# Performance work log

Measured on AMD Instinct MI355X. Metric: run time of the kernel, lower is better.

The kernel has to match this reference:

```python
import jax, jax.numpy as jnp
import numpy as np

B, C, VC, H, W = 4, 256, 128, 64, 64


def setup_inputs() -> dict:
    key = jax.random.key(0)
    kx, kq, kk, kv = jax.random.split(key, 4)
    # Conv2d 1x1 no-bias weights are just [out_channels, in_channels] matrices.
    s = 1.0 / np.sqrt(C)
    return {
        "x": jax.random.normal(kx, (B, C, H, W), dtype=jnp.float32),
        "Wq": jax.random.uniform(kq, (VC, C), minval=-s, maxval=s, dtype=jnp.float32),
        "Wk": jax.random.uniform(kk, (VC, C), minval=-s, maxval=s, dtype=jnp.float32),
        "Wv": jax.random.uniform(kv, (VC, C), minval=-s, maxval=s, dtype=jnp.float32),
    }


def reference(x, Wq, Wk, Wv):
    # 1x1 convs == per-pixel channel GEMMs
    Q = jnp.einsum('bchw,dc->bdhw', x, Wq)  # [B, VC, H, W]
    K = jnp.einsum('bchw,dc->bdhw', x, Wk)
    V = jnp.einsum('bchw,dc->bdhw', x, Wv)
    b, d, h, w = Q.shape
    # affinity over all spatial pairs: [B, H, W, H, W]
    aff = jnp.einsum('bdij,bdkl->bijkl', Q, K).reshape(b, h, w, h * w)
    aff = jax.nn.softmax(aff, axis=3).reshape(b, h, w, h, w)
    # attention-weighted aggregation of values
    out = jnp.einsum('bijkl,bdkl->bdij', aff, V)  # [B, VC, H, W]
    return out
```

## Files before the change

kernel.cpp:

```cpp
#include <hip/hip_runtime.h>
#include <hip/hip_bf16.h>

#define B_ 4
#define C_ 256
#define D_ 128
#define N_ 4096

typedef float f32x4 __attribute__((ext_vector_type(4)));
typedef short bf16x8 __attribute__((ext_vector_type(8)));
typedef short s16x4 __attribute__((ext_vector_type(4)));
typedef unsigned short u16;
typedef unsigned int u32;

__device__ __forceinline__ u16 f2bf(float f) {
  unsigned u = __float_as_uint(f);
  u += 0x7fffu + ((u >> 16) & 1u);
  return (u16)(u >> 16);
}
__device__ __forceinline__ float bf2f(u16 v) {
  return __uint_as_float(((u32)v) << 16);
}
__device__ __forceinline__ u32 cvt_pk_bf16(float a, float b) {
  u32 r;
  asm("v_cvt_pk_bf16_f32 %0, %1, %2" : "=v"(r) : "v"(a), "v"(b));
  return r;
}

__global__ __launch_bounds__(256) void castw_kernel(
    const float* __restrict__ Wq, const float* __restrict__ Wk,
    const float* __restrict__ Wv, u16* __restrict__ Whi,
    u16* __restrict__ Wlo) {
  const int i = blockIdx.x * 256 + threadIdx.x;
  const int m = i >> 13;
  const int j = (i & 8191) * 4;
  const float* src = (m == 0) ? Wq : (m == 1) ? Wk : Wv;
  const float scale = (m == 0) ? 1.44269504f : 1.0f;
  const float4 v = *(const float4*)(src + j);
  const float vv[4] = {v.x * scale, v.y * scale, v.z * scale, v.w * scale};
  s16x4 h, l;
#pragma unroll
  for (int k = 0; k < 4; ++k) {
    const u16 hb = f2bf(vv[k]);
    h[k] = (short)hb;
    l[k] = (short)f2bf(vv[k] - bf2f(hb));
  }
  *(s16x4*)&Whi[m * 32768 + j] = h;
  *(s16x4*)&Wlo[m * 32768 + j] = l;
}

__global__ __launch_bounds__(256, 3) void proj_kernel(
    const float* __restrict__ x, const u16* __restrict__ Whi,
    const u16* __restrict__ Wlo, u16* __restrict__ Qo, u16* __restrict__ Ko,
    u16* __restrict__ Vt) {
  __shared__ __align__(16) u16 xs_h[32 * 256];
  __shared__ __align__(16) u16 xs_l[32 * 256];

  const int n0 = blockIdx.x * 32;
  const int b = blockIdx.y;
  const int z = blockIdx.z;
  const int t = threadIdx.x;
  const int w = t >> 6, lane = t & 63, g = lane >> 4, c = lane & 15;

  {
    const float* xb = x + ((size_t)b * C_) * N_ + n0;
#pragma unroll
    for (int r = 0; r < 8; ++r) {
      const int id = r * 256 + t;
      const int cr = id >> 3, nq = (id & 7) * 4;
      const float4 v = *(const float4*)(xb + (size_t)cr * N_ + nq);
      const float vv[4] = {v.x, v.y, v.z, v.w};
#pragma unroll
      for (int k2 = 0; k2 < 4; ++k2) {
        const int idx2 = (nq + k2) * 256 + (cr ^ (((nq + k2) & 7) << 3));
        const u16 hb = f2bf(vv[k2]);
        xs_h[idx2] = hb;
        xs_l[idx2] = f2bf(vv[k2] - bf2f(hb));
      }
    }
  }
  __syncthreads();

  if (w < 2) {
    const size_t wo = (size_t)w * 32768;
    u16* __restrict__ O = (w == 0 ? Qo : Ko) + (size_t)b * N_ * D_;
#pragma unroll 1
    for (int dti = 0; dti < 4; ++dti) {
      const int dt = z * 4 + dti;
      f32x4 a0 = {0.f, 0.f, 0.f, 0.f};
      f32x4 a1 = {0.f, 0.f, 0.f, 0.f};
#pragma unroll 1
      for (int kcb = 0; kcb < 2; ++kcb) {
        bf16x8 wfh[4], wfl[4];
#pragma unroll
        for (int j = 0; j < 4; ++j) {
          const size_t off = wo + (size_t)(dt * 16 + c) * 256 +
                             (kcb * 4 + j) * 32 + g * 8;
          wfh[j] = *(const bf16x8*)&Whi[off];
          wfl[j] = *(const bf16x8*)&Wlo[off];
        }
#pragma unroll
        for (int j = 0; j < 4; ++j) {
          const int kc = kcb * 4 + j;
          const int col = (kc * 32 + g * 8) ^ ((c & 7) << 3);
          const bf16x8 xh0 = *(const bf16x8*)&xs_h[c * 256 + col];
          const bf16x8 xl0 = *(const bf16x8*)&xs_l[c * 256 + col];
          const bf16x8 xh1 = *(const bf16x8*)&xs_h[(16 + c) * 256 + col];
          const bf16x8 xl1 = *(const bf16x8*)&xs_l[(16 + c) * 256 + col];
          a0 = __builtin_amdgcn_mfma_f32_16x16x32_bf16(xh0, wfh[j], a0, 0, 0, 0);
          a0 = __builtin_amdgcn_mfma_f32_16x16x32_bf16(xh0, wfl[j], a0, 0, 0, 0);
          a0 = __builtin_amdgcn_mfma_f32_16x16x32_bf16(xl0, wfh[j], a0, 0, 0, 0);
          a1 = __builtin_amdgcn_mfma_f32_16x16x32_bf16(xh1, wfh[j], a1, 0, 0, 0);
          a1 = __builtin_amdgcn_mfma_f32_16x16x32_bf16(xh1, wfl[j], a1, 0, 0, 0);
          a1 = __builtin_amdgcn_mfma_f32_16x16x32_bf16(xl1, wfh[j], a1, 0, 0, 0);
        }
      }
#pragma unroll
      for (int i = 0; i < 4; ++i) {
        O[(size_t)(n0 + g * 4 + i) * D_ + dt * 16 + c] = f2bf(a0[i]);
        O[(size_t)(n0 + 16 + g * 4 + i) * D_ + dt * 16 + c] = f2bf(a1[i]);
      }
    }
  } else {
    const size_t wo = (size_t)2 * 32768;
    const int d0 = (w - 2) * 64 + z * 32;
    u16* __restrict__ O = Vt + (size_t)b * D_ * N_;
#pragma unroll 1
    for (int dti = 0; dti < 2; ++dti) {
      const int dr = d0 + dti * 16;
      f32x4 a0 = {0.f, 0.f, 0.f, 0.f};
      f32x4 a1 = {0.f, 0.f, 0.f, 0.f};
#pragma unroll 1
      for (int kcb = 0; kcb < 2; ++kcb) {
        bf16x8 wfh[4], wfl[4];
#pragma unroll
        for (int j = 0; j < 4; ++j) {
          const size_t off =
              wo + (size_t)(dr + c) * 256 + (kcb * 4 + j) * 32 + g * 8;
          wfh[j] = *(const bf16x8*)&Whi[off];
          wfl[j] = *(const bf16x8*)&Wlo[off];
        }
#pragma unroll
        for (int j = 0; j < 4; ++j) {
          const int kc = kcb * 4 + j;
          const int col = (kc * 32 + g * 8) ^ ((c & 7) << 3);
          const bf16x8 xh0 = *(const bf16x8*)&xs_h[c * 256 + col];
          const bf16x8 xl0 = *(const bf16x8*)&xs_l[c * 256 + col];
          const bf16x8 xh1 = *(const bf16x8*)&xs_h[(16 + c) * 256 + col];
          const bf16x8 xl1 = *(const bf16x8*)&xs_l[(16 + c) * 256 + col];
          a0 = __builtin_amdgcn_mfma_f32_16x16x32_bf16(wfh[j], xh0, a0, 0, 0, 0);
          a0 = __builtin_amdgcn_mfma_f32_16x16x32_bf16(wfl[j], xh0, a0, 0, 0, 0);
          a0 = __builtin_amdgcn_mfma_f32_16x16x32_bf16(wfh[j], xl0, a0, 0, 0, 0);
          a1 = __builtin_amdgcn_mfma_f32_16x16x32_bf16(wfh[j], xh1, a1, 0, 0, 0);
          a1 = __builtin_amdgcn_mfma_f32_16x16x32_bf16(wfl[j], xh1, a1, 0, 0, 0);
          a1 = __builtin_amdgcn_mfma_f32_16x16x32_bf16(wfh[j], xl1, a1, 0, 0, 0);
        }
      }
#pragma unroll
      for (int i = 0; i < 4; ++i) {
        O[(size_t)(dr + g * 4 + i) * N_ + n0 + c] = f2bf(a0[i]);
        O[(size_t)(dr + g * 4 + i) * N_ + n0 + 16 + c] = f2bf(a1[i]);
      }
    }
  }
}

__device__ __forceinline__ int kIdx(int row, int col) {
  return row * 128 + (col ^ ((row & 7) << 3));
}
__device__ __forceinline__ int vIdx(int d, int col) {
  return d * 64 + (col ^ ((d & 7) << 3));
}
__device__ __forceinline__ int kprm(int q) {
  const int ct = q >> 2, qq = q & 3;
  return ((ct >> 1) << 5) +
         (((qq >> 1) == (ct & 1)) ? (qq << 3) : (((qq ^ 2) << 3) + 4));
}

__global__ __launch_bounds__(256, 2) void attn_kernel(
    const u16* __restrict__ Q, const u16* __restrict__ K,
    const u16* __restrict__ Vt, u16* __restrict__ op,
    float* __restrict__ mb, float* __restrict__ lb,
    float* __restrict__ outf, int qt, int rem, int S) {
  __shared__ __align__(16) u16 lds_k[2][64 * 128];
  __shared__ __align__(16) u16 lds_vt[2][128 * 64];

  const int L = blockIdx.x;
  int qx, b, sid;
  if (((B_ * S) & 7) == 0) {
    const int gpx = (B_ * S) >> 3;
    const int xcd = L & 7, idx = L >> 3;
    const int grp = xcd * gpx + (idx >> 5);
    qx = idx & 31;
    b = grp / S;
    sid = grp - b * S;
  } else {
    qx = L & 31;
    const int r2 = L >> 5;
    b = r2 % B_;
    sid = r2 / B_;
  }
  const int q0 = qx * 128;
  const int NT = qt + (sid < rem ? 1 : 0);
  const int t0 = sid * qt + (sid < rem ? sid : rem);
  const int k0 = t0 * 64;
  const int t = threadIdx.x;
  const int w = t >> 6, lane = t & 63, g = lane >> 4, c = lane & 15;
  const int qw = q0 + w * 32;
  const bool ghi = (g & 2) != 0;

  const u16* __restrict__ Qb = Q + (size_t)b * N_ * D_;
  const u16* __restrict__ Kb = K + (size_t)b * N_ * D_;
  const u16* __restrict__ Vb = Vt + (size_t)b * D_ * N_;

  bf16x8 qf[2][4];
#pragma unroll
  for (int qh = 0; qh < 2; ++qh)
#pragma unroll
    for (int kc = 0; kc < 4; ++kc)
      qf[qh][kc] =
          *(const bf16x8*)&Qb[(size_t)(qw + qh * 16 + c) * D_ + kc * 32 + g * 8];

  f32x4 acc[8][2];
  f32x4 accl[2];
#pragma unroll
  for (int dt = 0; dt < 8; ++dt)
#pragma unroll
    for (int qh = 0; qh < 2; ++qh) acc[dt][qh] = (f32x4){0.f, 0.f, 0.f, 0.f};
  accl[0] = (f32x4){0.f, 0.f, 0.f, 0.f};
  accl[1] = (f32x4){0.f, 0.f, 0.f, 0.f};
  float mrow[2] = {-3.0e38f, -3.0e38f};
  const float THR = 11.5415603f;

  bf16x8 onesv;
#pragma unroll
  for (int j = 0; j < 8; ++j) onesv[j] = (short)0x3F80;

  bf16x8 krg[8], vrg[8];
  auto load_pair = [&](int kbase) {
#pragma unroll
    for (int h = 0; h < 2; ++h)
#pragma unroll
      for (int i = 0; i < 4; ++i) {
        const int idx = i * 256 + t;
        const int kb2 = kbase + h * 64;
        krg[h * 4 + i] =
            *(const bf16x8*)&Kb[(size_t)(kb2 + (idx >> 4)) * D_ + (idx & 15) * 8];
        vrg[h * 4 + i] =
            *(const bf16x8*)&Vb[(size_t)(idx >> 3) * N_ + kb2 + (idx & 7) * 8];
      }
  };
  load_pair(k0);

  auto proc = [&](const u16* kb, const u16* vb) {
    f32x4 s[4][2];
#pragma unroll
    for (int ct = 0; ct < 4; ++ct)
#pragma unroll
      for (int qh = 0; qh < 2; ++qh) s[ct][qh] = (f32x4){0.f, 0.f, 0.f, 0.f};
    __builtin_amdgcn_s_setprio(1);
#pragma unroll
    for (int kc = 0; kc < 4; ++kc) {
#pragma unroll
      for (int ct = 0; ct < 4; ++ct) {
        const bf16x8 kf = *(const bf16x8*)&kb[kIdx(ct * 16 + c, kc * 32 + g * 8)];
        s[ct][0] = __builtin_amdgcn_mfma_f32_16x16x32_bf16(kf, qf[0][kc], s[ct][0], 0, 0, 0);
        s[ct][1] = __builtin_amdgcn_mfma_f32_16x16x32_bf16(kf, qf[1][kc], s[ct][1], 0, 0, 0);
      }
    }
    __builtin_amdgcn_s_setprio(0);

    float pml[2];
#pragma unroll
    for (int qh = 0; qh < 2; ++qh) {
      const float m0 = fmaxf(fmaxf(s[0][qh][0], s[0][qh][1]),
                             fmaxf(s[0][qh][2], s[0][qh][3]));
      const float m1 = fmaxf(fmaxf(s[1][qh][0], s[1][qh][1]),
                             fmaxf(s[1][qh][2], s[1][qh][3]));
      const float m2 = fmaxf(fmaxf(s[2][qh][0], s[2][qh][1]),
                             fmaxf(s[2][qh][2], s[2][qh][3]));
      const float m3 = fmaxf(fmaxf(s[3][qh][0], s[3][qh][1]),
                             fmaxf(s[3][qh][2], s[3][qh][3]));
      pml[qh] = fmaxf(fmaxf(m0, m1), fmaxf(m2, m3));
    }
    const bool need =
        __any((pml[0] > mrow[0] + THR) || (pml[1] > mrow[1] + THR));
    if (need) {
#pragma unroll
      for (int qh = 0; qh < 2; ++qh) {
        float p = pml[qh];
        p = fmaxf(p, __shfl_xor(p, 16));
        p = fmaxf(p, __shfl_xor(p, 32));
        const float mnew = fmaxf(mrow[qh], p);
        const float scl = exp2f(mrow[qh] - mnew);
        mrow[qh] = mnew;
        accl[qh][0] *= scl; accl[qh][1] *= scl;
        accl[qh][2] *= scl; accl[qh][3] *= scl;
#pragma unroll
        for (int dt = 0; dt < 8; ++dt) {
          acc[dt][qh][0] *= scl; acc[dt][qh][1] *= scl;
          acc[dt][qh][2] *= scl; acc[dt][qh][3] *= scl;
        }
      }
    }
#pragma unroll
    for (int qh = 0; qh < 2; ++qh)
#pragma unroll
      for (int ct = 0; ct < 4; ++ct)
#pragma unroll
        for (int i = 0; i < 4; ++i)
          s[ct][qh][i] = exp2f(s[ct][qh][i] - mrow[qh]);

    u32 pfw[2][2][4];
#pragma unroll
    for (int kc = 0; kc < 2; ++kc) {
#pragma unroll
      for (int qh = 0; qh < 2; ++qh) {
        const u32 lo0 = cvt_pk_bf16(s[kc * 2][qh][0], s[kc * 2][qh][1]);
        const u32 lo1 = cvt_pk_bf16(s[kc * 2][qh][2], s[kc * 2][qh][3]);
        const u32 hi0 = cvt_pk_bf16(s[kc * 2 + 1][qh][0], s[kc * 2 + 1][qh][1]);
        const u32 hi1 = cvt_pk_bf16(s[kc * 2 + 1][qh][2], s[kc * 2 + 1][qh][3]);
        pfw[kc][qh][0] = ghi ? hi0 : lo0;
        pfw[kc][qh][1] = ghi ? hi1 : lo1;
        const u32 s0 = ghi ? lo0 : hi0;
        const u32 s1 = ghi ? lo1 : hi1;
        pfw[kc][qh][2] = (u32)__shfl_xor((int)s0, 32);
        pfw[kc][qh][3] = (u32)__shfl_xor((int)s1, 32);
      }
    }

#pragma unroll
    for (int kc = 0; kc < 2; ++kc) {
      union { u32 w2[4]; bf16x8 v; } u0, u1;
#pragma unroll
      for (int j = 0; j < 4; ++j) { u0.w2[j] = pfw[kc][0][j]; u1.w2[j] = pfw[kc][1][j]; }
      __builtin_amdgcn_s_setprio(1);
      accl[0] = __builtin_amdgcn_mfma_f32_16x16x32_bf16(onesv, u0.v, accl[0], 0, 0, 0);
      accl[1] = __builtin_amdgcn_mfma_f32_16x16x32_bf16(onesv, u1.v, accl[1], 0, 0, 0);
#pragma unroll
      for (int dt = 0; dt < 8; ++dt) {
        const bf16x8 vf = *(const bf16x8*)&vb[vIdx(dt * 16 + c, kc * 32 + g * 8)];
        acc[dt][0] = __builtin_amdgcn_mfma_f32_16x16x32_bf16(vf, u0.v, acc[dt][0], 0, 0, 0);
        acc[dt][1] = __builtin_amdgcn_mfma_f32_16x16x32_bf16(vf, u1.v, acc[dt][1], 0, 0, 0);
      }
      __builtin_amdgcn_s_setprio(0);
    }
  };

  for (int kt = 0; kt < NT; kt += 2) {
    __syncthreads();
#pragma unroll
    for (int h = 0; h < 2; ++h)
#pragma unroll
      for (int i = 0; i < 4; ++i) {
        const int idx = i * 256 + t;
        *(bf16x8*)&lds_k[h][kIdx(idx >> 4, (idx & 15) * 8)] = krg[h * 4 + i];
        const int d = idx >> 3, rc = idx & 7;
        const bf16x8 vv = vrg[h * 4 + i];
        s16x4 lo, hi;
        lo[0] = vv[0]; lo[1] = vv[1]; lo[2] = vv[2]; lo[3] = vv[3];
        hi[0] = vv[4]; hi[1] = vv[5]; hi[2] = vv[6]; hi[3] = vv[7];
        *(s16x4*)&lds_vt[h][vIdx(d, kprm(rc * 2))] = lo;
        *(s16x4*)&lds_vt[h][vIdx(d, kprm(rc * 2 + 1))] = hi;
      }
    if (kt + 2 < NT) load_pair(k0 + (kt + 2) * 64);
    __syncthreads();

    proc(&lds_k[0][0], &lds_vt[0][0]);
    proc(&lds_k[1][0], &lds_vt[1][0]);
  }

#pragma unroll
  for (int qh = 0; qh < 2; ++qh) {
    const int n = qw + qh * 16 + c;
    const float lr = accl[qh][0];
    if (mb) {
      u16* __restrict__ ob = op + ((size_t)(sid * B_ + b) * D_) * N_;
#pragma unroll
      for (int dt = 0; dt < 8; ++dt)
#pragma unroll
        for (int i = 0; i < 4; ++i)
          ob[(size_t)(dt * 16 + g * 4 + i) * N_ + n] = f2bf(acc[dt][qh][i]);
      if (g == 0) {
        mb[(size_t)(sid * B_ + b) * N_ + n] = mrow[qh];
        lb[(size_t)(sid * B_ + b) * N_ + n] = lr;
      }
    } else {
      const float linv = 1.0f / lr;
      float* __restrict__ ob = outf + (size_t)b * D_ * N_;
#pragma unroll
      for (int dt = 0; dt < 8; ++dt)
#pragma unroll
        for (int i = 0; i < 4; ++i)
          ob[(size_t)(dt * 16 + g * 4 + i) * N_ + n] = acc[dt][qh][i] * linv;
    }
  }
}

__global__ __launch_bounds__(256) void combine_kernel(
    const u16* __restrict__ op, const float* __restrict__ mbu,
    const float* __restrict__ lbu, float* __restrict__ out, int S) {
  const int idx = blockIdx.x * 256 + threadIdx.x;
  const int n0 = (idx & (N_ / 4 - 1)) * 4;
  const int bd = idx >> 10;
  const int b = bd >> 7, d = bd & (D_ - 1);

  float4 msv[8], lsv[8];
  float M0 = -3e38f, M1 = -3e38f, M2 = -3e38f, M3 = -3e38f;
#pragma unroll
  for (int s = 0; s < 8; ++s)
    if (s < S) {
      msv[s] = *(const float4*)&mbu[(size_t)(s * B_ + b) * N_ + n0];
      lsv[s] = *(const float4*)&lbu[(size_t)(s * B_ + b) * N_ + n0];
      M0 = fmaxf(M0, msv[s].x); M1 = fmaxf(M1, msv[s].y);
      M2 = fmaxf(M2, msv[s].z); M3 = fmaxf(M3, msv[s].w);
    }
  float d0 = 0.f, d1 = 0.f, d2 = 0.f, d3 = 0.f;
  float a0 = 0.f, a1 = 0.f, a2 = 0.f, a3 = 0.f;
#pragma unroll
  for (int s = 0; s < 8; ++s)
    if (s < S) {
      const float w0 = exp2f(msv[s].x - M0);
      const float w1 = exp2f(msv[s].y - M1);
      const float w2 = exp2f(msv[s].z - M2);
      const float w3 = exp2f(msv[s].w - M3);
      d0 += lsv[s].x * w0; d1 += lsv[s].y * w1;
      d2 += lsv[s].z * w2; d3 += lsv[s].w * w3;
      const s16x4 o =
          *(const s16x4*)&op[((size_t)(s * B_ + b) * D_ + d) * N_ + n0];
      a0 += w0 * bf2f((u16)o[0]); a1 += w1 * bf2f((u16)o[1]);
      a2 += w2 * bf2f((u16)o[2]); a3 += w3 * bf2f((u16)o[3]);
    }
  float4 r = {a0 / d0, a1 / d1, a2 / d2, a3 / d3};
  *(float4*)&out[((size_t)b * D_ + d) * N_ + n0] = r;
}

extern "C" void kernel_launch(void* const* d_in, const int* in_sizes, int n_in,
                              void* d_out, int out_size, void* d_ws, size_t ws_size,
                              hipStream_t stream) {
  const float* x  = (const float*)d_in[0];
  const float* Wq = (const float*)d_in[1];
  const float* Wk = (const float*)d_in[2];
  const float* Wv = (const float*)d_in[3];
  float* out = (float*)d_out;

  u16* whi  = (u16*)d_ws;
  u16* wlo  = whi + (size_t)3 * 128 * 256;
  u16* q_ws = wlo + (size_t)3 * 128 * 256;
  u16* k_ws = q_ws + (size_t)B_ * N_ * D_;
  u16* v_ws = k_ws + (size_t)B_ * N_ * D_;

  castw_kernel<<<96, 256, 0, stream>>>(Wq, Wk, Wv, whi, wlo);
  proj_kernel<<<dim3(N_ / 32, B_, 2), 256, 0, stream>>>(x, whi, wlo, q_ws,
                                                        k_ws, v_ws);

  const size_t baseB =
      ((size_t)6 * 128 * 256 + (size_t)3 * B_ * N_ * D_) * 2;
  int S = 0;
  const int cands[3] = {4, 2, 1};
  for (int ci = 0; ci < 3; ++ci) {
    const int cand = cands[ci];
    const size_t need = baseB + (size_t)cand * ((size_t)B_ * D_ * N_ * 2 +
                                                (size_t)2 * B_ * N_ * 4);
    if (ws_size >= need) { S = cand; break; }
  }
  if (S > 1) {
    u16* opb = (u16*)((char*)d_ws + baseB);
    float* mbuf = (float*)(opb + (size_t)S * B_ * D_ * N_);
    float* lbuf = mbuf + (size_t)S * B_ * N_;
    attn_kernel<<<dim3(32 * B_ * S), 256, 0, stream>>>(
        q_ws, k_ws, v_ws, opb, mbuf, lbuf, nullptr, 64 / S, 64 % S, S);
    combine_kernel<<<(B_ * D_ * N_ / 4) / 256, 256, 0, stream>>>(opb, mbuf,
                                                                 lbuf, out, S);
  } else {
    attn_kernel<<<dim3(32 * B_), 256, 0, stream>>>(
        q_ws, k_ws, v_ws, nullptr, nullptr, nullptr, out, 64, 0, 1);
  }
}
```

Before: 96.68 us.

## Split x cast/transpose into separate kernel and restructure projection loops

```diff
diff --git a/kernel.cpp b/kernel.cpp
--- a/kernel.cpp
+++ b/kernel.cpp
@@ -48,10 +48,53 @@
   *(s16x4*)&Wlo[m * 32768 + j] = l;
 }
 
-__global__ __launch_bounds__(256, 3) void proj_kernel(
-    const float* __restrict__ x, const u16* __restrict__ Whi,
-    const u16* __restrict__ Wlo, u16* __restrict__ Qo, u16* __restrict__ Ko,
-    u16* __restrict__ Vt) {
+__global__ __launch_bounds__(256) void castx_kernel(
+    const float* __restrict__ x, u16* __restrict__ xthi,
+    u16* __restrict__ xtlo) {
+  __shared__ u32 hl[64 * 69];
+
+  const int n0 = blockIdx.x * 64;
+  const int c0 = blockIdx.y * 64;
+  const int b = blockIdx.z;
+  const int t = threadIdx.x;
+
+#pragma unroll
+  for (int r = 0; r < 4; ++r) {
+    const int id = r * 256 + t;
+    const int cr = id >> 4, nq = (id & 15) * 4;
+    const float4 v =
+        *(const float4*)(x + ((size_t)(b * C_ + c0 + cr)) * N_ + n0 + nq);
+    const float vv[4] = {v.x, v.y, v.z, v.w};
+#pragma unroll
+    for (int k = 0; k < 4; ++k) {
+      const u16 hb = f2bf(vv[k]);
+      const u16 lb = f2bf(vv[k] - bf2f(hb));
+      hl[cr * 69 + nq + k] = ((u32)hb << 16) | (u32)lb;
+    }
+  }
+  __syncthreads();
+
+  const int nr = t >> 2, cb = (t & 3) * 16;
+  u32 vj[16];
+#pragma unroll
+  for (int j = 0; j < 16; ++j) vj[j] = hl[(cb + j) * 69 + nr];
+  bf16x8 h0, h1, l0, l1;
+#pragma unroll
+  for (int j = 0; j < 8; ++j) {
+    h0[j] = (short)(vj[j] >> 16);      l0[j] = (short)(vj[j] & 0xffff);
+    h1[j] = (short)(vj[8 + j] >> 16);  l1[j] = (short)(vj[8 + j] & 0xffff);
+  }
+  const size_t off = ((size_t)b * N_ + n0 + nr) * 256 + c0 + cb;
+  *(bf16x8*)&xthi[off] = h0;
+  *(bf16x8*)&xthi[off + 8] = h1;
+  *(bf16x8*)&xtlo[off] = l0;
+  *(bf16x8*)&xtlo[off + 8] = l1;
+}
+
+__global__ __launch_bounds__(256, 4) void proj_kernel(
+    const u16* __restrict__ xthi, const u16* __restrict__ xtlo,
+    const u16* __restrict__ Whi, const u16* __restrict__ Wlo,
+    u16* __restrict__ Qo, u16* __restrict__ Ko, u16* __restrict__ Vt) {
   __shared__ __align__(16) u16 xs_h[32 * 256];
   __shared__ __align__(16) u16 xs_l[32 * 256];
 
@@ -60,105 +103,110 @@
   const int z = blockIdx.z;
   const int t = threadIdx.x;
   const int w = t >> 6, lane = t & 63, g = lane >> 4, c = lane & 15;
+  const int role = (w + blockIdx.x) & 3;
 
   {
-    const float* xb = x + ((size_t)b * C_) * N_ + n0;
-#pragma unroll
-    for (int r = 0; r < 8; ++r) {
-      const int id = r * 256 + t;
-      const int cr = id >> 3, nq = (id & 7) * 4;
-      const float4 v = *(const float4*)(xb + (size_t)cr * N_ + nq);
-      const float vv[4] = {v.x, v.y, v.z, v.w};
-#pragma unroll
-      for (int k2 = 0; k2 < 4; ++k2) {
-        const int idx2 = (nq + k2) * 256 + (cr ^ (((nq + k2) & 7) << 3));
-        const u16 hb = f2bf(vv[k2]);
-        xs_h[idx2] = hb;
-        xs_l[idx2] = f2bf(vv[k2] - bf2f(hb));
-      }
+    const size_t base = ((size_t)b * N_ + n0) * 256;
+#pragma unroll
+    for (int i = 0; i < 4; ++i) {
+      const int id = i * 256 + t;
+      const int n = id >> 5, c8 = (id & 31) * 8;
+      const int li = n * 256 + (c8 ^ ((n & 7) << 3));
+      *(bf16x8*)&xs_h[li] = *(const bf16x8*)&xthi[base + n * 256 + c8];
+      *(bf16x8*)&xs_l[li] = *(const bf16x8*)&xtlo[base + n * 256 + c8];
     }
   }
   __syncthreads();
 
-  if (w < 2) {
-    const size_t wo = (size_t)w * 32768;
-    u16* __restrict__ O = (w == 0 ? Qo : Ko) + (size_t)b * N_ * D_;
+  if (role < 2) {
+    const size_t wo = (size_t)role * 32768;
+    u16* __restrict__ O = (role == 0 ? Qo : Ko) + (size_t)b * N_ * D_;
 #pragma unroll 1
-    for (int dti = 0; dti < 4; ++dti) {
-      const int dt = z * 4 + dti;
-      f32x4 a0 = {0.f, 0.f, 0.f, 0.f};
-      f32x4 a1 = {0.f, 0.f, 0.f, 0.f};
-#pragma unroll 1
+    for (int nt = 0; nt < 2; ++nt) {
+      f32x4 a[4];
+#pragma unroll
+      for (int dti = 0; dti < 4; ++dti) a[dti] = (f32x4){0.f, 0.f, 0.f, 0.f};
+#pragma unroll
       for (int kcb = 0; kcb < 2; ++kcb) {
-        bf16x8 wfh[4], wfl[4];
-#pragma unroll
-        for (int j = 0; j < 4; ++j) {
-          const size_t off = wo + (size_t)(dt * 16 + c) * 256 +
-                             (kcb * 4 + j) * 32 + g * 8;
-          wfh[j] = *(const bf16x8*)&Whi[off];
-          wfl[j] = *(const bf16x8*)&Wlo[off];
+        bf16x8 xh[4], xl[4];
+#pragma unroll
+        for (int jj = 0; jj < 4; ++jj) {
+          const int col = (((kcb * 4 + jj) * 32) + g * 8) ^ ((c & 7) << 3);
+          xh[jj] = *(const bf16x8*)&xs_h[(nt * 16 + c) * 256 + col];
+          xl[jj] = *(const bf16x8*)&xs_l[(nt * 16 + c) * 256 + col];
         }
 #pragma unroll
-        for (int j = 0; j < 4; ++j) {
-          const int kc = kcb * 4 + j;
-          const int col = (kc * 32 + g * 8) ^ ((c & 7) << 3);
-          const bf16x8 xh0 = *(const bf16x8*)&xs_h[c * 256 + col];
-          const bf16x8 xl0 = *(const bf16x8*)&xs_l[c * 256 + col];
-          const bf16x8 xh1 = *(const bf16x8*)&xs_h[(16 + c) * 256 + col];
-          const bf16x8 xl1 = *(const bf16x8*)&xs_l[(16 + c) * 256 + col];
-          a0 = __builtin_amdgcn_mfma_f32_16x16x32_bf16(xh0, wfh[j], a0, 0, 0, 0);
-          a0 = __builtin_amdgcn_mfma_f32_16x16x32_bf16(xh0, wfl[j], a0, 0, 0, 0);
-          a0 = __builtin_amdgcn_mfma_f32_16x16x32_bf16(xl0, wfh[j], a0, 0, 0, 0);
-          a1 = __builtin_amdgcn_mfma_f32_16x16x32_bf16(xh1, wfh[j], a1, 0, 0, 0);
-          a1 = __builtin_amdgcn_mfma_f32_16x16x32_bf16(xh1, wfl[j], a1, 0, 0, 0);
-          a1 = __builtin_amdgcn_mfma_f32_16x16x32_bf16(xl1, wfh[j], a1, 0, 0, 0);
+        for (int dti = 0; dti < 4; ++dti) {
+          const int dt = z * 4 + dti;
+          bf16x8 wh[4], wl[4];
+#pragma unroll
+          for (int jj = 0; jj < 4; ++jj) {
+            const size_t off = wo + (size_t)(dt * 16 + c) * 256 +
+                               (kcb * 4 + jj) * 32 + g * 8;
+            wh[jj] = *(const bf16x8*)&Whi[off];
+            wl[jj] = *(const bf16x8*)&Wlo[off];
+          }
+#pragma unroll
+          for (int jj = 0; jj < 4; ++jj) {
+            a[dti] = __builtin_amdgcn_mfma_f32_16x16x32_bf16(xh[jj], wh[jj], a[dti], 0, 0, 0);
+            a[dti] = __builtin_amdgcn_mfma_f32_16x16x32_bf16(xh[jj], wl[jj], a[dti], 0, 0, 0);
+            a[dti] = __builtin_amdgcn_mfma_f32_16x16x32_bf16(xl[jj], wh[jj], a[dti], 0, 0, 0);
+          }
         }
       }
 #pragma unroll
-      for (int i = 0; i < 4; ++i) {
-        O[(size_t)(n0 + g * 4 + i) * D_ + dt * 16 + c] = f2bf(a0[i]);
-        O[(size_t)(n0 + 16 + g * 4 + i) * D_ + dt * 16 + c] = f2bf(a1[i]);
+      for (int dti = 0; dti < 4; ++dti) {
+        const int dt = z * 4 + dti;
+#pragma unroll
+        for (int i = 0; i < 4; ++i)
+          O[(size_t)(n0 + nt * 16 + g * 4 + i) * D_ + dt * 16 + c] =
+              f2bf(a[dti][i]);
       }
     }
   } else {
     const size_t wo = (size_t)2 * 32768;
-    const int d0 = (w - 2) * 64 + z * 32;
+    const int d0 = (role - 2) * 64 + z * 32;
     u16* __restrict__ O = Vt + (size_t)b * D_ * N_;
 #pragma unroll 1
-    for (int dti = 0; dti < 2; ++dti) {
-      const int dr = d0 + dti * 16;
-      f32x4 a0 = {0.f, 0.f, 0.f, 0.f};
-      f32x4 a1 = {0.f, 0.f, 0.f, 0.f};
-#pragma unroll 1
+    for (int nt = 0; nt < 2; ++nt) {
+      f32x4 a[2];
+      a[0] = (f32x4){0.f, 0.f, 0.f, 0.f};
+      a[1] = (f32x4){0.f, 0.f, 0.f, 0.f};
+#pragma unroll
       for (int kcb = 0; kcb < 2; ++kcb) {
-        bf16x8 wfh[4], wfl[4];
-#pragma unroll
-        for (int j = 0; j < 4; ++j) {
-          const size_t off =
-              wo + (size_t)(dr + c) * 256 + (kcb * 4 + j) * 32 + g * 8;
-          wfh[j] = *(const bf16x8*)&Whi[off];
-          wfl[j] = *(const bf16x8*)&Wlo[off];
+        bf16x8 xh[4], xl[4];
+#pragma unroll
+        for (int jj = 0; jj < 4; ++jj) {
+          const int col = (((kcb * 4 + jj) * 32) + g * 8) ^ ((c & 7) << 3);
+          xh[jj] = *(const bf16x8*)&xs_h[(nt * 16 + c) * 256 + col];
+          xl[jj] = *(const bf16x8*)&xs_l[(nt * 16 + c) * 256 + col];
         }
 #pragma unroll
-        for (int j = 0; j < 4; ++j) {
-          const int kc = kcb * 4 + j;
-          const int col = (kc * 32 + g * 8) ^ ((c & 7) << 3);
-          const bf16x8 xh0 = *(const bf16x8*)&xs_h[c * 256 + col];
-          const bf16x8 xl0 = *(const bf16x8*)&xs_l[c * 256 + col];
-          const bf16x8 xh1 = *(const bf16x8*)&xs_h[(16 + c) * 256 + col];
-          const bf16x8 xl1 = *(const bf16x8*)&xs_l[(16 + c) * 256 + col];
-          a0 = __builtin_amdgcn_mfma_f32_16x16x32_bf16(wfh[j], xh0, a0, 0, 0, 0);
-          a0 = __builtin_amdgcn_mfma_f32_16x16x32_bf16(wfl[j], xh0, a0, 0, 0, 0);
-          a0 = __builtin_amdgcn_mfma_f32_16x16x32_bf16(wfh[j], xl0, a0, 0, 0, 0);
-          a1 = __builtin_amdgcn_mfma_f32_16x16x32_bf16(wfh[j], xh1, a1, 0, 0, 0);
-          a1 = __builtin_amdgcn_mfma_f32_16x16x32_bf16(wfl[j], xh1, a1, 0, 0, 0);
-          a1 = __builtin_amdgcn_mfma_f32_16x16x32_bf16(wfh[j], xl1, a1, 0, 0, 0);
+        for (int dti = 0; dti < 2; ++dti) {
+          const int dr = d0 + dti * 16;
+          bf16x8 wh[4], wl[4];
+#pragma unroll
+          for (int jj = 0; jj < 4; ++jj) {
+            const size_t off =
+                wo + (size_t)(dr + c) * 256 + (kcb * 4 + jj) * 32 + g * 8;
+            wh[jj] = *(const bf16x8*)&Whi[off];
+            wl[jj] = *(const bf16x8*)&Wlo[off];
+          }
+#pragma unroll
+          for (int jj = 0; jj < 4; ++jj) {
+            a[dti] = __builtin_amdgcn_mfma_f32_16x16x32_bf16(wh[jj], xh[jj], a[dti], 0, 0, 0);
+            a[dti] = __builtin_amdgcn_mfma_f32_16x16x32_bf16(wl[jj], xh[jj], a[dti], 0, 0, 0);
+            a[dti] = __builtin_amdgcn_mfma_f32_16x16x32_bf16(wh[jj], xl[jj], a[dti], 0, 0, 0);
+          }
         }
       }
 #pragma unroll
-      for (int i = 0; i < 4; ++i) {
-        O[(size_t)(dr + g * 4 + i) * N_ + n0 + c] = f2bf(a0[i]);
-        O[(size_t)(dr + g * 4 + i) * N_ + n0 + 16 + c] = f2bf(a1[i]);
+      for (int dti = 0; dti < 2; ++dti) {
+        const int dr = d0 + dti * 16;
+#pragma unroll
+        for (int i = 0; i < 4; ++i)
+          O[(size_t)(dr + g * 4 + i) * N_ + n0 + nt * 16 + c] =
+              f2bf(a[dti][i]);
       }
     }
   }
@@ -445,16 +493,19 @@
 
   u16* whi  = (u16*)d_ws;
   u16* wlo  = whi + (size_t)3 * 128 * 256;
-  u16* q_ws = wlo + (size_t)3 * 128 * 256;
+  u16* xthi = wlo + (size_t)3 * 128 * 256;
+  u16* xtlo = xthi + (size_t)B_ * N_ * C_;
+  u16* q_ws = xtlo + (size_t)B_ * N_ * C_;
   u16* k_ws = q_ws + (size_t)B_ * N_ * D_;
   u16* v_ws = k_ws + (size_t)B_ * N_ * D_;
 
   castw_kernel<<<96, 256, 0, stream>>>(Wq, Wk, Wv, whi, wlo);
-  proj_kernel<<<dim3(N_ / 32, B_, 2), 256, 0, stream>>>(x, whi, wlo, q_ws,
-                                                        k_ws, v_ws);
-
-  const size_t baseB =
-      ((size_t)6 * 128 * 256 + (size_t)3 * B_ * N_ * D_) * 2;
+  castx_kernel<<<dim3(N_ / 64, C_ / 64, B_), 256, 0, stream>>>(x, xthi, xtlo);
+  proj_kernel<<<dim3(N_ / 32, B_, 2), 256, 0, stream>>>(xthi, xtlo, whi, wlo,
+                                                        q_ws, k_ws, v_ws);
+
+  const size_t baseB = ((size_t)6 * 128 * 256 + (size_t)2 * B_ * N_ * C_ +
+                        (size_t)3 * B_ * N_ * D_) * 2;
   int S = 0;
   const int cands[3] = {4, 2, 1};
   for (int ci = 0; ci < 3; ++ci) {
```

Result: slower. 140.9 us (+45.7%).
